# Kernel tuning notes

Hardware: AMD Instinct MI355X
Metric: run time of the kernel (lower is better)

Reference implementation:

```python
import jax, jax.numpy as jnp
import numpy as np

N_NODES = 100000
N_EDGES = 3200000


def gcn_conv(x, edge_index, W, b, num_nodes):
    """PyG GCNConv: x' = D^{-1/2} (A + I) D^{-1/2} (x W) + b (symmetric norm, self-loops)."""
    x = x @ W  # [N, out]
    loop = jnp.arange(num_nodes, dtype=edge_index.dtype)
    src = jnp.concatenate([edge_index[0], loop])
    dst = jnp.concatenate([edge_index[1], loop])
    # degree over destination nodes (incl. self loops)
    deg = jax.ops.segment_sum(jnp.ones_like(dst, dtype=x.dtype), dst, num_segments=num_nodes)
    dinv = jnp.where(deg > 0, jax.lax.rsqrt(deg), 0.0)
    norm = dinv[src] * dinv[dst]  # [E + N]
    msg = x[src] * norm[:, None]  # gather + scale
    out = jax.ops.segment_sum(msg, dst, num_segments=num_nodes)  # scatter-add
    return out + b


def setup_inputs() -> dict:
    key = jax.random.key(0)
    k = jax.random.split(key, 5)
    x = jax.random.normal(k[0], (N_NODES, 256), dtype=jnp.float32)
    edge_index = jax.random.randint(k[1], (2, N_EDGES), 0, N_NODES, dtype=jnp.int64)
    W1 = jax.random.normal(k[2], (256, 16), dtype=jnp.float32) * (1.0 / np.sqrt(256))
    b1 = jnp.zeros((16,), dtype=jnp.float32)
    W2 = jax.random.normal(k[3], (16, 8), dtype=jnp.float32) * (1.0 / np.sqrt(16))
    b2 = jnp.zeros((8,), dtype=jnp.float32)
    return {"x": x, "edge_index": edge_index, "W1": W1, "b1": b1, "W2": W2, "b2": b2}


def reference(x, edge_index, W1, b1, W2, b2):
    n = x.shape[0]
    h = gcn_conv(x, edge_index, W1, b1, n)
    h = jax.nn.relu(h)
    # dropout is identity in eval mode (training=False)
    h = gcn_conv(h, edge_index, W2, b2, n)
    return jax.nn.log_softmax(h, axis=1)
```

## Files before the change

kernel.cpp:

```cpp
#include <hip/hip_runtime.h>

#define NN 100000
#define NE 3200000
#define NB 391
#define CAP 9216
#define PB 16
#define CH_A (256 * PB)

typedef _Float16 half4 __attribute__((ext_vector_type(4)));
typedef _Float16 half8 __attribute__((ext_vector_type(8)));

__device__ __forceinline__ float4 f4fma(float s, float4 a, float4 c) {
  c.x = fmaf(s, a.x, c.x); c.y = fmaf(s, a.y, c.y);
  c.z = fmaf(s, a.z, c.z); c.w = fmaf(s, a.w, c.w);
  return c;
}

template<int CTRL>
__device__ __forceinline__ float4 quad_bcast(float4 v) {
  float4 r;
  r.x = __int_as_float(__builtin_amdgcn_update_dpp(__float_as_int(v.x), __float_as_int(v.x), CTRL, 0xF, 0xF, false));
  r.y = __int_as_float(__builtin_amdgcn_update_dpp(__float_as_int(v.y), __float_as_int(v.y), CTRL, 0xF, 0xF, false));
  r.z = __int_as_float(__builtin_amdgcn_update_dpp(__float_as_int(v.z), __float_as_int(v.z), CTRL, 0xF, 0xF, false));
  r.w = __int_as_float(__builtin_amdgcn_update_dpp(__float_as_int(v.w), __float_as_int(v.w), CTRL, 0xF, 0xF, false));
  return r;
}

__device__ __forceinline__ int edge_val(const int* __restrict__ ei, int idx, bool w64) {
  return w64 ? ei[2 * idx] : ei[idx];
}

__global__ __launch_bounds__(512) void init_kernel(const int* __restrict__ ei,
                                                   int* __restrict__ bucket_cursor,
                                                   int* __restrict__ flag) {
  int t = threadIdx.x;
  if (t < NB) bucket_cursor[t] = 0;
  if (t == 511) {
    int o = 0;
    for (int i = 1; i < 64; i += 2) o |= ei[i];
    *flag = (o == 0) ? 1 : 0;
  }
}

__global__ __launch_bounds__(256) void bin_kernel(const int* __restrict__ ei,
                                                  int* __restrict__ bucket_cursor,
                                                  int* __restrict__ pairs,
                                                  const int* __restrict__ flag) {
  __shared__ int  cnt[4][NB];
  __shared__ int  wcur[4][NB];
  __shared__ int  lbase[NB];
  __shared__ int  gbase[NB];
  __shared__ int  sc[512];
  __shared__ int2 stage[CH_A];
  int t = threadIdx.x;
  int wv = t >> 6;
  for (int k = t; k < 4 * NB; k += 256) (&cnt[0][0])[k] = 0;
  __syncthreads();
  bool w64 = (*flag != 0);
  int base = blockIdx.x * CH_A;
  int nval = min(CH_A, NE - base);
  int s[PB], d[PB];
#pragma unroll
  for (int i = 0; i < PB; ++i) {
    int e = base + i * 256 + t;
    if (e < NE) {
      s[i] = edge_val(ei, e, w64);
      d[i] = edge_val(ei, NE + e, w64);
      atomicAdd(&cnt[wv][d[i] >> 8], 1);
    } else {
      d[i] = -1;
    }
  }
  __syncthreads();
  int tA = (t < NB) ? cnt[0][t] + cnt[1][t] + cnt[2][t] + cnt[3][t] : 0;
  int tB = (t + 256 < NB) ? cnt[0][t + 256] + cnt[1][t + 256] + cnt[2][t + 256] + cnt[3][t + 256] : 0;
  sc[t] = tA; sc[t + 256] = tB;
  __syncthreads();
#pragma unroll
  for (int off = 1; off < 512; off <<= 1) {
    int u0 = (t >= off) ? sc[t - off] : 0;
    int u1 = (t + 256 >= off) ? sc[t + 256 - off] : 0;
    __syncthreads();
    sc[t] += u0; sc[t + 256] += u1;
    __syncthreads();
  }
#pragma unroll
  for (int h = 0; h < 2; ++h) {
    int k = t + h * 256;
    if (k < NB) {
      int tot = (h == 0) ? tA : tB;
      int lb = sc[k] - tot;
      lbase[k] = lb;
      gbase[k] = (tot > 0) ? atomicAdd(&bucket_cursor[k], tot) : 0;
      int c0 = cnt[0][k], c1 = cnt[1][k], c2 = cnt[2][k];
      wcur[0][k] = lb;
      wcur[1][k] = lb + c0;
      wcur[2][k] = lb + c0 + c1;
      wcur[3][k] = lb + c0 + c1 + c2;
    }
  }
  __syncthreads();
#pragma unroll
  for (int i = 0; i < PB; ++i) {
    if (d[i] >= 0) {
      int b = d[i] >> 8;
      int slot = atomicAdd(&wcur[wv][b], 1);
      stage[slot] = make_int2(s[i], d[i]);
    }
  }
  __syncthreads();
  for (int k = t; k < nval; k += 256) {
    int2 p = stage[k];
    int b = p.y >> 8;
    pairs[(size_t)b * CAP + gbase[b] + (k - lbase[b])] = p.x | ((p.y & 255) << 24);
  }
}

__global__ __launch_bounds__(256) void bscan_kernel(const int* __restrict__ bucket_cursor,
                                                    int* __restrict__ bucket_scan) {
  __shared__ int sc[512];
  __shared__ int orig[512];
  int t = threadIdx.x;
  int v0 = (t < NB) ? bucket_cursor[t] : 0;
  int v1 = (t + 256 < NB) ? bucket_cursor[t + 256] : 0;
  sc[t] = v0; orig[t] = v0;
  sc[t + 256] = v1; orig[t + 256] = v1;
  __syncthreads();
#pragma unroll
  for (int off = 1; off < 512; off <<= 1) {
    int u0 = (t >= off) ? sc[t - off] : 0;
    int u1 = (t + 256 >= off) ? sc[t + 256 - off] : 0;
    __syncthreads();
    sc[t] += u0; sc[t + 256] += u1;
    __syncthreads();
  }
  if (t < NB) bucket_scan[t] = sc[t] - orig[t];
  if (t + 256 < NB) bucket_scan[t + 256] = sc[t + 256] - orig[t + 256];
}

__global__ __launch_bounds__(512) void sort_kernel(const int* __restrict__ pairs,
                                                   const int* __restrict__ bucket_cursor,
                                                   const int* __restrict__ bucket_scan,
                                                   int* __restrict__ srt,
                                                   int* __restrict__ deg,
                                                   int* __restrict__ row_ofs,
                                                   float* __restrict__ dinv) {
  __shared__ int hist[256];
  __shared__ int sc[256];
  __shared__ int cur[256];
  int t = threadIdx.x;
  int b = blockIdx.x;
  int cnt_b = bucket_cursor[b];
  size_t in_base = (size_t)b * CAP;
  int out_base = bucket_scan[b];
  if (t < 256) hist[t] = 0;
  __syncthreads();
  for (int i = t; i < cnt_b; i += 512) {
    int pk = pairs[in_base + i];
    atomicAdd(&hist[((unsigned)pk) >> 24], 1);
  }
  __syncthreads();
  if (t < 256) sc[t] = hist[t];
  __syncthreads();
#pragma unroll
  for (int off = 1; off < 256; off <<= 1) {
    int u = (t < 256 && t >= off) ? sc[t - off] : 0;
    __syncthreads();
    if (t < 256) sc[t] += u;
    __syncthreads();
  }
  if (t < 256) {
    int excl = sc[t] - hist[t];
    cur[t] = out_base + excl;
    int n = b * 256 + t;
    if (n < NN) {
      deg[n] = hist[t];
      row_ofs[n] = out_base + excl;
      dinv[n] = rsqrtf((float)hist[t] + 1.0f);
    }
  }
  __syncthreads();
  for (int i = t; i < cnt_b; i += 512) {
    int pk = pairs[in_base + i];
    int pos = atomicAdd(&cur[((unsigned)pk) >> 24], 1);
    srt[pos] = pk & 0xFFFFFF;
  }
}

__global__ __launch_bounds__(256) void gemm1_kernel(const float* __restrict__ x,
                                                    const float* __restrict__ W1,
                                                    const float* __restrict__ dinv,
                                                    _Float16* __restrict__ xw1h) {
  const int lane = threadIdx.x & 63;
  const int wv   = threadIdx.x >> 6;
  const int node0 = (blockIdx.x * 4 + wv) * 8;
  const int cg = lane >> 2;
  const int jl = lane & 3;
  float4 w[16];
#pragma unroll
  for (int k = 0; k < 4; ++k)
#pragma unroll
    for (int c = 0; c < 4; ++c)
      w[k * 4 + c] = *(const float4*)(W1 + (cg * 16 + k * 4 + c) * 16 + jl * 4);
  float4 xv[8];
#pragma unroll
  for (int i = 0; i < 8; ++i)
    xv[i] = *(const float4*)(x + (size_t)(node0 + i) * 256 + lane * 4);
  float4 acc[8];
#pragma unroll
  for (int i = 0; i < 8; ++i) acc[i] = make_float4(0.f, 0.f, 0.f, 0.f);
#pragma unroll
  for (int i = 0; i < 8; ++i) {
    float4 b = quad_bcast<0x00>(xv[i]);
    acc[i] = f4fma(b.x, w[0], acc[i]);  acc[i] = f4fma(b.y, w[1], acc[i]);
    acc[i] = f4fma(b.z, w[2], acc[i]);  acc[i] = f4fma(b.w, w[3], acc[i]);
  }
#pragma unroll
  for (int i = 0; i < 8; ++i) {
    float4 b = quad_bcast<0x55>(xv[i]);
    acc[i] = f4fma(b.x, w[4], acc[i]);  acc[i] = f4fma(b.y, w[5], acc[i]);
    acc[i] = f4fma(b.z, w[6], acc[i]);  acc[i] = f4fma(b.w, w[7], acc[i]);
  }
#pragma unroll
  for (int i = 0; i < 8; ++i) {
    float4 b = quad_bcast<0xAA>(xv[i]);
    acc[i] = f4fma(b.x, w[8], acc[i]);  acc[i] = f4fma(b.y, w[9], acc[i]);
    acc[i] = f4fma(b.z, w[10], acc[i]); acc[i] = f4fma(b.w, w[11], acc[i]);
  }
#pragma unroll
  for (int i = 0; i < 8; ++i) {
    float4 b = quad_bcast<0xFF>(xv[i]);
    acc[i] = f4fma(b.x, w[12], acc[i]); acc[i] = f4fma(b.y, w[13], acc[i]);
    acc[i] = f4fma(b.z, w[14], acc[i]); acc[i] = f4fma(b.w, w[15], acc[i]);
  }
#pragma unroll
  for (int m = 4; m <= 32; m <<= 1) {
#pragma unroll
    for (int i = 0; i < 8; ++i) {
      acc[i].x += __shfl_xor(acc[i].x, m);
      acc[i].y += __shfl_xor(acc[i].y, m);
      acc[i].z += __shfl_xor(acc[i].z, m);
      acc[i].w += __shfl_xor(acc[i].w, m);
    }
  }
  if (lane < 4) {
#pragma unroll
    for (int i = 0; i < 8; ++i) {
      float dn = dinv[node0 + i];
      float4 a = acc[i];
      half4 hv;
      hv[0] = (_Float16)(a.x * dn); hv[1] = (_Float16)(a.y * dn);
      hv[2] = (_Float16)(a.z * dn); hv[3] = (_Float16)(a.w * dn);
      *(half4*)(xw1h + (size_t)(node0 + i) * 16 + lane * 4) = hv;
    }
  }
}

__global__ __launch_bounds__(256) void layer1_kernel(const int* __restrict__ srt,
                                                     const int* __restrict__ row_ofs,
                                                     const int* __restrict__ deg,
                                                     const float* __restrict__ dinv,
                                                     const _Float16* __restrict__ xw1h,
                                                     const float* __restrict__ W2,
                                                     const float* __restrict__ b1,
                                                     _Float16* __restrict__ h1w2h) {
  int t = blockIdx.x * 256 + threadIdx.x;
  int n = t >> 4, sub = t & 15, q = sub & 3, e = sub >> 2;
  if (n >= NN) return;
  int base = row_ofs[n], cnt = deg[n];
  float4 acc = make_float4(0.f, 0.f, 0.f, 0.f);
  int s_next = (e < cnt) ? srt[base + e] : 0;
  for (int i = e; i < cnt; i += 4) {
    int s = s_next;
    if (i + 4 < cnt) s_next = srt[base + i + 4];
    half4 v = *(const half4*)(xw1h + (size_t)s * 16 + q * 4);
    acc.x += (float)v[0]; acc.y += (float)v[1];
    acc.z += (float)v[2]; acc.w += (float)v[3];
  }
#pragma unroll
  for (int m = 4; m <= 8; m <<= 1) {
    acc.x += __shfl_xor(acc.x, m);
    acc.y += __shfl_xor(acc.y, m);
    acc.z += __shfl_xor(acc.z, m);
    acc.w += __shfl_xor(acc.w, m);
  }
  float dn = dinv[n];
  half4 svh = *(const half4*)(xw1h + (size_t)n * 16 + q * 4);
  float4 bv = *(const float4*)(b1 + q * 4);
  float h[4];
  h[0] = fmaxf(fmaf(dn, acc.x + (float)svh[0], bv.x), 0.f);
  h[1] = fmaxf(fmaf(dn, acc.y + (float)svh[1], bv.y), 0.f);
  h[2] = fmaxf(fmaf(dn, acc.z + (float)svh[2], bv.z), 0.f);
  h[3] = fmaxf(fmaf(dn, acc.w + (float)svh[3], bv.w), 0.f);
  float p[8] = {0.f, 0.f, 0.f, 0.f, 0.f, 0.f, 0.f, 0.f};
  const float4* W2v = (const float4*)W2;
#pragma unroll
  for (int f = 0; f < 4; ++f) {
    float4 wlo = W2v[(q * 4 + f) * 2];
    float4 whi = W2v[(q * 4 + f) * 2 + 1];
    p[0] = fmaf(h[f], wlo.x, p[0]); p[1] = fmaf(h[f], wlo.y, p[1]);
    p[2] = fmaf(h[f], wlo.z, p[2]); p[3] = fmaf(h[f], wlo.w, p[3]);
    p[4] = fmaf(h[f], whi.x, p[4]); p[5] = fmaf(h[f], whi.y, p[5]);
    p[6] = fmaf(h[f], whi.z, p[6]); p[7] = fmaf(h[f], whi.w, p[7]);
  }
#pragma unroll
  for (int m = 1; m <= 2; m <<= 1)
#pragma unroll
    for (int j = 0; j < 8; ++j)
      p[j] += __shfl_xor(p[j], m);
  if (sub == 0) {
    half8 hv;
#pragma unroll
    for (int j = 0; j < 8; ++j) hv[j] = (_Float16)(p[j] * dn);
    *(half8*)(h1w2h + (size_t)n * 8) = hv;
  }
}

__global__ __launch_bounds__(256) void layer2_kernel(const int* __restrict__ srt,
                                                     const int* __restrict__ row_ofs,
                                                     const int* __restrict__ deg,
                                                     const float* __restrict__ dinv,
                                                     const _Float16* __restrict__ h1w2h,
                                                     const float* __restrict__ b2,
                                                     float* __restrict__ out) {
  int t = blockIdx.x * 256 + threadIdx.x;
  int n = t >> 3, sub = t & 7, q = sub & 1, e = sub >> 1;
  if (n >= NN) return;
  int base = row_ofs[n], cnt = deg[n];
  float4 acc = make_float4(0.f, 0.f, 0.f, 0.f);
  int s_next = (e < cnt) ? srt[base + e] : 0;
  for (int i = e; i < cnt; i += 4) {
    int s = s_next;
    if (i + 4 < cnt) s_next = srt[base + i + 4];
    half4 v = *(const half4*)(h1w2h + (size_t)s * 8 + q * 4);
    acc.x += (float)v[0]; acc.y += (float)v[1];
    acc.z += (float)v[2]; acc.w += (float)v[3];
  }
#pragma unroll
  for (int m = 2; m <= 4; m <<= 1) {
    acc.x += __shfl_xor(acc.x, m);
    acc.y += __shfl_xor(acc.y, m);
    acc.z += __shfl_xor(acc.z, m);
    acc.w += __shfl_xor(acc.w, m);
  }
  float dn = dinv[n];
  half4 svh = *(const half4*)(h1w2h + (size_t)n * 8 + q * 4);
  float4 bv = *(const float4*)(b2 + q * 4);
  float4 v;
  v.x = fmaf(dn, acc.x + (float)svh[0], bv.x);
  v.y = fmaf(dn, acc.y + (float)svh[1], bv.y);
  v.z = fmaf(dn, acc.z + (float)svh[2], bv.z);
  v.w = fmaf(dn, acc.w + (float)svh[3], bv.w);
  float mh = fmaxf(fmaxf(v.x, v.y), fmaxf(v.z, v.w));
  float m = fmaxf(mh, __shfl_xor(mh, 1));
  float se = expf(v.x - m) + expf(v.y - m) + expf(v.z - m) + expf(v.w - m);
  float st = se + __shfl_xor(se, 1);
  float ls = m + logf(st);
  if (sub < 2)
    *(float4*)(out + (size_t)n * 8 + q * 4) = make_float4(v.x - ls, v.y - ls, v.z - ls, v.w - ls);
}

extern "C" void kernel_launch(void* const* d_in, const int* in_sizes, int n_in,
                              void* d_out, int out_size, void* d_ws, size_t ws_size,
                              hipStream_t stream) {
  const float* x  = (const float*)d_in[0];
  const int*   ei = (const int*)d_in[1];
  const float* W1 = (const float*)d_in[2];
  const float* b1 = (const float*)d_in[3];
  const float* W2 = (const float*)d_in[4];
  const float* b2 = (const float*)d_in[5];
  float* out = (float*)d_out;

  int*      pairs = (int*)d_ws;
  _Float16* xw1h  = (_Float16*)(pairs + (size_t)NB * CAP);
  _Float16* h1w2h = xw1h + (size_t)16 * NN;
  float*    dinv  = (float*)(h1w2h + (size_t)8 * NN);
  int*      deg   = (int*)(dinv + NN);
  int*      row_ofs = deg + NN;
  int*      srt   = row_ofs + NN;
  int*      bucket_cursor = srt + NE;
  int*      bucket_scan   = bucket_cursor + NB + 1;
  int*      flag          = bucket_scan + NB + 1;

  init_kernel<<<1, 512, 0, stream>>>(ei, bucket_cursor, flag);
  bin_kernel<<<(NE + CH_A - 1) / CH_A, 256, 0, stream>>>(ei, bucket_cursor, pairs, flag);
  bscan_kernel<<<1, 256, 0, stream>>>(bucket_cursor, bucket_scan);
  sort_kernel<<<NB, 512, 0, stream>>>(pairs, bucket_cursor, bucket_scan, srt, deg, row_ofs, dinv);
  gemm1_kernel<<<NN / 32, 256, 0, stream>>>(x, W1, dinv, xw1h);
  layer1_kernel<<<(16 * NN + 255) / 256, 256, 0, stream>>>(srt, row_ofs, deg, dinv, xw1h, W2, b1, h1w2h);
  layer2_kernel<<<(8 * NN + 255) / 256, 256, 0, stream>>>(srt, row_ofs, deg, dinv, h1w2h, b2, out);
}
```

Before: 319.6 us.

## Fuse bucket scan into sort, inline dtype flag, and widen gather loads

The int64 detection moves into bin_kernel as a per-block wave ballot, and the 64-bit path reads edge pairs with int4 vector loads. The separate bucket scan kernel is removed; each sort block computes its own prefix from bucket_cursor with a wave reduction, and it uses two histogram copies to spread LDS atomic contention. Layer1 and layer2 now assign fewer threads per node and use half8 loads, which halves the thread count and the shuffle reductions. The aim is to cut launch count and per-edge overhead, at the cost of more registers per thread and less parallelism in the gather.

```diff
diff --git a/kernel.cpp b/kernel.cpp
--- a/kernel.cpp
+++ b/kernel.cpp
@@ -26,49 +26,60 @@
   return r;
 }
 
-__device__ __forceinline__ int edge_val(const int* __restrict__ ei, int idx, bool w64) {
-  return w64 ? ei[2 * idx] : ei[idx];
-}
-
-__global__ __launch_bounds__(512) void init_kernel(const int* __restrict__ ei,
-                                                   int* __restrict__ bucket_cursor,
-                                                   int* __restrict__ flag) {
+__global__ __launch_bounds__(512) void init_kernel(int* __restrict__ bucket_cursor) {
   int t = threadIdx.x;
   if (t < NB) bucket_cursor[t] = 0;
-  if (t == 511) {
-    int o = 0;
-    for (int i = 1; i < 64; i += 2) o |= ei[i];
-    *flag = (o == 0) ? 1 : 0;
-  }
 }
 
 __global__ __launch_bounds__(256) void bin_kernel(const int* __restrict__ ei,
                                                   int* __restrict__ bucket_cursor,
-                                                  int* __restrict__ pairs,
-                                                  const int* __restrict__ flag) {
+                                                  int* __restrict__ pairs) {
   __shared__ int  cnt[4][NB];
   __shared__ int  wcur[4][NB];
   __shared__ int  lbase[NB];
   __shared__ int  gbase[NB];
   __shared__ int  sc[512];
   __shared__ int2 stage[CH_A];
+  __shared__ int  w64flag;
   int t = threadIdx.x;
   int wv = t >> 6;
   for (int k = t; k < 4 * NB; k += 256) (&cnt[0][0])[k] = 0;
-  __syncthreads();
-  bool w64 = (*flag != 0);
+  if (t < 64) {
+    int o = (t < 32) ? ei[2 * t + 1] : 0;
+    unsigned long long bl = __ballot(o != 0);
+    if (t == 0) w64flag = (bl == 0ULL) ? 1 : 0;
+  }
+  __syncthreads();
+  bool w64 = (w64flag != 0);
   int base = blockIdx.x * CH_A;
   int nval = min(CH_A, NE - base);
   int s[PB], d[PB];
-#pragma unroll
-  for (int i = 0; i < PB; ++i) {
-    int e = base + i * 256 + t;
-    if (e < NE) {
-      s[i] = edge_val(ei, e, w64);
-      d[i] = edge_val(ei, NE + e, w64);
-      atomicAdd(&cnt[wv][d[i] >> 8], 1);
-    } else {
-      d[i] = -1;
+  if (w64) {
+#pragma unroll
+    for (int i = 0; i < 8; ++i) {
+      int e0 = base + i * 512 + 2 * t;
+      if (e0 < NE) {
+        int4 svv = *(const int4*)(ei + 2 * (size_t)e0);
+        int4 dvv = *(const int4*)(ei + 2 * (size_t)NE + 2 * (size_t)e0);
+        s[2 * i] = svv.x; s[2 * i + 1] = svv.z;
+        d[2 * i] = dvv.x; d[2 * i + 1] = dvv.z;
+        atomicAdd(&cnt[wv][dvv.x >> 8], 1);
+        atomicAdd(&cnt[wv][dvv.z >> 8], 1);
+      } else {
+        d[2 * i] = -1; d[2 * i + 1] = -1;
+      }
+    }
+  } else {
+#pragma unroll
+    for (int i = 0; i < PB; ++i) {
+      int e = base + i * 256 + t;
+      if (e < NE) {
+        s[i] = ei[e];
+        d[i] = ei[NE + e];
+        atomicAdd(&cnt[wv][d[i] >> 8], 1);
+      } else {
+        d[i] = -1;
+      }
     }
   }
   __syncthreads();
@@ -116,51 +127,41 @@
   }
 }
 
-__global__ __launch_bounds__(256) void bscan_kernel(const int* __restrict__ bucket_cursor,
-                                                    int* __restrict__ bucket_scan) {
-  __shared__ int sc[512];
-  __shared__ int orig[512];
-  int t = threadIdx.x;
-  int v0 = (t < NB) ? bucket_cursor[t] : 0;
-  int v1 = (t + 256 < NB) ? bucket_cursor[t + 256] : 0;
-  sc[t] = v0; orig[t] = v0;
-  sc[t + 256] = v1; orig[t + 256] = v1;
-  __syncthreads();
-#pragma unroll
-  for (int off = 1; off < 512; off <<= 1) {
-    int u0 = (t >= off) ? sc[t - off] : 0;
-    int u1 = (t + 256 >= off) ? sc[t + 256 - off] : 0;
-    __syncthreads();
-    sc[t] += u0; sc[t + 256] += u1;
-    __syncthreads();
-  }
-  if (t < NB) bucket_scan[t] = sc[t] - orig[t];
-  if (t + 256 < NB) bucket_scan[t + 256] = sc[t + 256] - orig[t + 256];
-}
-
 __global__ __launch_bounds__(512) void sort_kernel(const int* __restrict__ pairs,
                                                    const int* __restrict__ bucket_cursor,
-                                                   const int* __restrict__ bucket_scan,
                                                    int* __restrict__ srt,
                                                    int* __restrict__ deg,
                                                    int* __restrict__ row_ofs,
                                                    float* __restrict__ dinv) {
-  __shared__ int hist[256];
+  __shared__ int hist[2][256];
   __shared__ int sc[256];
   __shared__ int cur[256];
+  __shared__ int wsum[8];
+  __shared__ int obase;
   int t = threadIdx.x;
   int b = blockIdx.x;
   int cnt_b = bucket_cursor[b];
   size_t in_base = (size_t)b * CAP;
-  int out_base = bucket_scan[b];
-  if (t < 256) hist[t] = 0;
-  __syncthreads();
+  if (t < 256) { hist[0][t] = 0; hist[1][t] = 0; }
+  int v = (t < b) ? bucket_cursor[t] : 0;
+#pragma unroll
+  for (int m = 1; m <= 32; m <<= 1) v += __shfl_xor(v, m);
+  if ((t & 63) == 0) wsum[t >> 6] = v;
+  __syncthreads();
+  if (t == 0) {
+    int s0 = 0;
+#pragma unroll
+    for (int k = 0; k < 8; ++k) s0 += wsum[k];
+    obase = s0;
+  }
+  int hsel = t >> 8;
   for (int i = t; i < cnt_b; i += 512) {
     int pk = pairs[in_base + i];
-    atomicAdd(&hist[((unsigned)pk) >> 24], 1);
-  }
-  __syncthreads();
-  if (t < 256) sc[t] = hist[t];
+    atomicAdd(&hist[hsel][((unsigned)pk) >> 24], 1);
+  }
+  __syncthreads();
+  int out_base = obase;
+  if (t < 256) sc[t] = hist[0][t] + hist[1][t];
   __syncthreads();
 #pragma unroll
   for (int off = 1; off < 256; off <<= 1) {
@@ -170,13 +171,14 @@
     __syncthreads();
   }
   if (t < 256) {
-    int excl = sc[t] - hist[t];
+    int tot = hist[0][t] + hist[1][t];
+    int excl = sc[t] - tot;
     cur[t] = out_base + excl;
     int n = b * 256 + t;
     if (n < NN) {
-      deg[n] = hist[t];
+      deg[n] = tot;
       row_ofs[n] = out_base + excl;
-      dinv[n] = rsqrtf((float)hist[t] + 1.0f);
+      dinv[n] = rsqrtf((float)tot + 1.0f);
     }
   }
   __syncthreads();
@@ -265,49 +267,44 @@
                                                      const float* __restrict__ b1,
                                                      _Float16* __restrict__ h1w2h) {
   int t = blockIdx.x * 256 + threadIdx.x;
-  int n = t >> 4, sub = t & 15, q = sub & 3, e = sub >> 2;
+  int n = t >> 3, sub = t & 7, q = sub & 1, e = sub >> 1;
   if (n >= NN) return;
   int base = row_ofs[n], cnt = deg[n];
-  float4 acc = make_float4(0.f, 0.f, 0.f, 0.f);
+  float acc[8] = {0.f, 0.f, 0.f, 0.f, 0.f, 0.f, 0.f, 0.f};
   int s_next = (e < cnt) ? srt[base + e] : 0;
   for (int i = e; i < cnt; i += 4) {
     int s = s_next;
     if (i + 4 < cnt) s_next = srt[base + i + 4];
-    half4 v = *(const half4*)(xw1h + (size_t)s * 16 + q * 4);
-    acc.x += (float)v[0]; acc.y += (float)v[1];
-    acc.z += (float)v[2]; acc.w += (float)v[3];
-  }
-#pragma unroll
-  for (int m = 4; m <= 8; m <<= 1) {
-    acc.x += __shfl_xor(acc.x, m);
-    acc.y += __shfl_xor(acc.y, m);
-    acc.z += __shfl_xor(acc.z, m);
-    acc.w += __shfl_xor(acc.w, m);
-  }
+    half8 v = *(const half8*)(xw1h + (size_t)s * 16 + q * 8);
+#pragma unroll
+    for (int j = 0; j < 8; ++j) acc[j] += (float)v[j];
+  }
+#pragma unroll
+  for (int m = 2; m <= 4; m <<= 1)
+#pragma unroll
+    for (int j = 0; j < 8; ++j) acc[j] += __shfl_xor(acc[j], m);
   float dn = dinv[n];
-  half4 svh = *(const half4*)(xw1h + (size_t)n * 16 + q * 4);
-  float4 bv = *(const float4*)(b1 + q * 4);
-  float h[4];
-  h[0] = fmaxf(fmaf(dn, acc.x + (float)svh[0], bv.x), 0.f);
-  h[1] = fmaxf(fmaf(dn, acc.y + (float)svh[1], bv.y), 0.f);
-  h[2] = fmaxf(fmaf(dn, acc.z + (float)svh[2], bv.z), 0.f);
-  h[3] = fmaxf(fmaf(dn, acc.w + (float)svh[3], bv.w), 0.f);
+  half8 sv = *(const half8*)(xw1h + (size_t)n * 16 + q * 8);
+  float bb[8];
+  *(float4*)bb       = *(const float4*)(b1 + q * 8);
+  *(float4*)(bb + 4) = *(const float4*)(b1 + q * 8 + 4);
+  float h[8];
+#pragma unroll
+  for (int j = 0; j < 8; ++j)
+    h[j] = fmaxf(fmaf(dn, acc[j] + (float)sv[j], bb[j]), 0.f);
   float p[8] = {0.f, 0.f, 0.f, 0.f, 0.f, 0.f, 0.f, 0.f};
   const float4* W2v = (const float4*)W2;
 #pragma unroll
-  for (int f = 0; f < 4; ++f) {
-    float4 wlo = W2v[(q * 4 + f) * 2];
-    float4 whi = W2v[(q * 4 + f) * 2 + 1];
+  for (int f = 0; f < 8; ++f) {
+    float4 wlo = W2v[(q * 8 + f) * 2];
+    float4 whi = W2v[(q * 8 + f) * 2 + 1];
     p[0] = fmaf(h[f], wlo.x, p[0]); p[1] = fmaf(h[f], wlo.y, p[1]);
     p[2] = fmaf(h[f], wlo.z, p[2]); p[3] = fmaf(h[f], wlo.w, p[3]);
     p[4] = fmaf(h[f], whi.x, p[4]); p[5] = fmaf(h[f], whi.y, p[5]);
     p[6] = fmaf(h[f], whi.z, p[6]); p[7] = fmaf(h[f], whi.w, p[7]);
   }
 #pragma unroll
-  for (int m = 1; m <= 2; m <<= 1)
-#pragma unroll
-    for (int j = 0; j < 8; ++j)
-      p[j] += __shfl_xor(p[j], m);
+  for (int j = 0; j < 8; ++j) p[j] += __shfl_xor(p[j], 1);
   if (sub == 0) {
     half8 hv;
 #pragma unroll
@@ -324,40 +321,43 @@
                                                      const float* __restrict__ b2,
                                                      float* __restrict__ out) {
   int t = blockIdx.x * 256 + threadIdx.x;
-  int n = t >> 3, sub = t & 7, q = sub & 1, e = sub >> 1;
+  int n = t >> 2, e = t & 3;
   if (n >= NN) return;
   int base = row_ofs[n], cnt = deg[n];
-  float4 acc = make_float4(0.f, 0.f, 0.f, 0.f);
+  float acc[8] = {0.f, 0.f, 0.f, 0.f, 0.f, 0.f, 0.f, 0.f};
   int s_next = (e < cnt) ? srt[base + e] : 0;
   for (int i = e; i < cnt; i += 4) {
     int s = s_next;
     if (i + 4 < cnt) s_next = srt[base + i + 4];
-    half4 v = *(const half4*)(h1w2h + (size_t)s * 8 + q * 4);
-    acc.x += (float)v[0]; acc.y += (float)v[1];
-    acc.z += (float)v[2]; acc.w += (float)v[3];
-  }
-#pragma unroll
-  for (int m = 2; m <= 4; m <<= 1) {
-    acc.x += __shfl_xor(acc.x, m);
-    acc.y += __shfl_xor(acc.y, m);
-    acc.z += __shfl_xor(acc.z, m);
-    acc.w += __shfl_xor(acc.w, m);
-  }
+    half8 v = *(const half8*)(h1w2h + (size_t)s * 8);
+#pragma unroll
+    for (int j = 0; j < 8; ++j) acc[j] += (float)v[j];
+  }
+#pragma unroll
+  for (int m = 1; m <= 2; m <<= 1)
+#pragma unroll
+    for (int j = 0; j < 8; ++j) acc[j] += __shfl_xor(acc[j], m);
   float dn = dinv[n];
-  half4 svh = *(const half4*)(h1w2h + (size_t)n * 8 + q * 4);
-  float4 bv = *(const float4*)(b2 + q * 4);
-  float4 v;
-  v.x = fmaf(dn, acc.x + (float)svh[0], bv.x);
-  v.y = fmaf(dn, acc.y + (float)svh[1], bv.y);
-  v.z = fmaf(dn, acc.z + (float)svh[2], bv.z);
-  v.w = fmaf(dn, acc.w + (float)svh[3], bv.w);
-  float mh = fmaxf(fmaxf(v.x, v.y), fmaxf(v.z, v.w));
-  float m = fmaxf(mh, __shfl_xor(mh, 1));
-  float se = expf(v.x - m) + expf(v.y - m) + expf(v.z - m) + expf(v.w - m);
-  float st = se + __shfl_xor(se, 1);
-  float ls = m + logf(st);
-  if (sub < 2)
-    *(float4*)(out + (size_t)n * 8 + q * 4) = make_float4(v.x - ls, v.y - ls, v.z - ls, v.w - ls);
+  half8 sv = *(const half8*)(h1w2h + (size_t)n * 8);
+  float bb[8];
+  *(float4*)bb       = *(const float4*)b2;
+  *(float4*)(bb + 4) = *(const float4*)(b2 + 4);
+  float v8[8];
+#pragma unroll
+  for (int j = 0; j < 8; ++j) v8[j] = fmaf(dn, acc[j] + (float)sv[j], bb[j]);
+  float mx = v8[0];
+#pragma unroll
+  for (int j = 1; j < 8; ++j) mx = fmaxf(mx, v8[j]);
+  float se = 0.f;
+#pragma unroll
+  for (int j = 0; j < 8; ++j) se += expf(v8[j] - mx);
+  float ls = mx + logf(se);
+  if (e < 2) {
+    float4 o4 = (e == 0)
+        ? make_float4(v8[0] - ls, v8[1] - ls, v8[2] - ls, v8[3] - ls)
+        : make_float4(v8[4] - ls, v8[5] - ls, v8[6] - ls, v8[7] - ls);
+    *(float4*)(out + (size_t)n * 8 + e * 4) = o4;
+  }
 }
 
 extern "C" void kernel_launch(void* const* d_in, const int* in_sizes, int n_in,
@@ -379,14 +379,11 @@
   int*      row_ofs = deg + NN;
   int*      srt   = row_ofs + NN;
   int*      bucket_cursor = srt + NE;
-  int*      bucket_scan   = bucket_cursor + NB + 1;
-  int*      flag          = bucket_scan + NB + 1;
-
-  init_kernel<<<1, 512, 0, stream>>>(ei, bucket_cursor, flag);
-  bin_kernel<<<(NE + CH_A - 1) / CH_A, 256, 0, stream>>>(ei, bucket_cursor, pairs, flag);
-  bscan_kernel<<<1, 256, 0, stream>>>(bucket_cursor, bucket_scan);
-  sort_kernel<<<NB, 512, 0, stream>>>(pairs, bucket_cursor, bucket_scan, srt, deg, row_ofs, dinv);
+
+  init_kernel<<<1, 512, 0, stream>>>(bucket_cursor);
+  bin_kernel<<<(NE + CH_A - 1) / CH_A, 256, 0, stream>>>(ei, bucket_cursor, pairs);
+  sort_kernel<<<NB, 512, 0, stream>>>(pairs, bucket_cursor, srt, deg, row_ofs, dinv);
   gemm1_kernel<<<NN / 32, 256, 0, stream>>>(x, W1, dinv, xw1h);
-  layer1_kernel<<<(16 * NN + 255) / 256, 256, 0, stream>>>(srt, row_ofs, deg, dinv, xw1h, W2, b1, h1w2h);
-  layer2_kernel<<<(8 * NN + 255) / 256, 256, 0, stream>>>(srt, row_ofs, deg, dinv, h1w2h, b2, out);
-}
+  layer1_kernel<<<(8 * NN + 255) / 256, 256, 0, stream>>>(srt, row_ofs, deg, dinv, xw1h, W2, b1, h1w2h);
+  layer2_kernel<<<(4 * NN + 255) / 256, 256, 0, stream>>>(srt, row_ofs, deg, dinv, h1w2h, b2, out);
+}
```

After: 306.3 us. 1.04x faster.
